# Performance work log

Measured on AMD Instinct MI355X. Metric: run time of the kernel, lower is better.

Reference implementation:

```python
import jax, jax.numpy as jnp
import numpy as np

B, N, KNN_K = 4, 4096, 32
C1, C = 128, 256
K_SLOTS, RECON_M, N_RECON = 4, 96, 128
SLOT_ITERS = 3

def _ln(x, g, b):
    m = x.mean(-1, keepdims=True)
    v = jnp.var(x, axis=-1, keepdims=True)
    return (x - m) * jax.lax.rsqrt(v + 1e-5) * g + b

def _gather(f, idx):
    # f [B,P,C], idx [B,N,K] -> [B,N,K,C]
    return jax.vmap(lambda a, i: a[i])(f, idx)

def _knn(xyz, k):
    sq = jnp.sum(xyz * xyz, -1)
    d = sq[:, :, None] + sq[:, None, :] - 2.0 * jnp.einsum('bnc,bmc->bnm', xyz, xyz)
    return jax.lax.top_k(-d, k)[1]

def _conv_block(xyz, feats, W, b):
    # InterZPConv-style: KNN neighbor gather -> per-neighbor transform -> max aggregate
    idx = _knn(xyz, KNN_K)
    rel = _gather(xyz, idx) - xyz[:, :, None, :]
    h = jnp.concatenate([_gather(feats, idx), rel], axis=-1)
    h = jax.nn.relu(jnp.einsum('bnkc,cd->bnkd', h, W) + b)
    return h.max(axis=2)

def _bn(x, g, b):
    # BatchNorm2d (training mode) over (batch, slot) axes for 1x1-conv stacks
    m = x.mean(axis=(0, 1), keepdims=True)
    v = jnp.var(x, axis=(0, 1), keepdims=True)
    return (x - m) * jax.lax.rsqrt(v + 1e-5) * g + b

def _gru(upd, prev, W_ih, W_hh, b_ih, b_hh):
    gi = upd @ W_ih + b_ih
    gh = prev @ W_hh + b_hh
    r = jax.nn.sigmoid(gi[..., :C] + gh[..., :C])
    z = jax.nn.sigmoid(gi[..., C:2 * C] + gh[..., C:2 * C])
    n = jnp.tanh(gi[..., 2 * C:] + r * gh[..., 2 * C:])
    return (1.0 - z) * n + z * prev

def _chamfer(a, b):
    # a [B,M,3], b [B,P,3] -> (min over b per a-point, min over a per b-point), squared dists
    d = jnp.sum((a[..., :, None, :] - b[..., None, :, :]) ** 2, axis=-1)
    return d.min(axis=-1), d.min(axis=-2)

def _fps(pts):
    # farthest point sampling of N_RECON points from pts [P,3]
    P = pts.shape[0]
    d0 = jnp.full((P,), 1e10, pts.dtype)
    def step(carry, _):
        d, last = carry
        d = jnp.minimum(d, jnp.sum((pts - pts[last]) ** 2, axis=-1))
        nxt = jnp.argmax(d).astype(jnp.int32)
        return (d, nxt), nxt
    _, idxs = jax.lax.scan(step, (d0, jnp.array(0, jnp.int32)), None, length=N_RECON - 1)
    return jnp.concatenate([jnp.zeros((1,), jnp.int32), idxs])

def setup_inputs() -> dict:
    key = jax.random.key(0)
    ks = jax.random.split(key, 16)
    w = lambda k, s: jax.random.normal(k, s, jnp.float32) * 0.02
    z = lambda *s: jnp.zeros(s, jnp.float32)
    o = lambda *s: jnp.ones(s, jnp.float32)
    return {
        'x': jax.random.normal(ks[0], (B, 3, N), jnp.float32),
        'pose': jnp.zeros((B, N, 4, 4), jnp.float32),
        'W1': w(ks[1], (1 + 3, C1)), 'b1': z(C1),
        'W2': w(ks[2], (C1 + 3, C)), 'b2': z(C),
        'slots_mu': w(ks[3], (1, 1, C)), 'slots_sigma': jnp.abs(w(ks[4], (1, 1, C))) + 0.01,
        'ln_in_g': o(C), 'ln_in_b': z(C),
        'ln_slot_g': o(C), 'ln_slot_b': z(C),
        'ln_ff_g': o(C), 'ln_ff_b': z(C),
        'Wq': w(ks[5], (C, C)), 'Wk': w(ks[6], (C, C)), 'Wv': w(ks[7], (C, C)),
        'W_ih': w(ks[8], (C, 3 * C)), 'W_hh': w(ks[9], (C, 3 * C)),
        'b_ih': z(3 * C), 'b_hh': z(3 * C),
        'Wm1': w(ks[10], (C, C)), 'bm1': z(C),
        'Wm2': w(ks[11], (C, C)), 'bm2': z(C),
        'Wr1': w(ks[12], (C, C)), 'br1': z(C), 'g1': o(C), 'be1': z(C),
        'Wr2': w(ks[13], (C, C)), 'br2': z(C), 'g2': o(C), 'be2': z(C),
        'Wr3': w(ks[14], (C, RECON_M * 3)), 'br3': z(RECON_M * 3),
    }

def reference(x, pose, W1, b1, W2, b2, slots_mu, slots_sigma, ln_in_g, ln_in_b,
              ln_slot_g, ln_slot_b, ln_ff_g, ln_ff_b, Wq, Wk, Wv,
              W_ih, W_hh, b_ih, b_hh, Wm1, bm1, Wm2, bm2,
              Wr1, br1, g1, be1, Wr2, br2, g2, be2, Wr3, br3):
    xyz = jnp.transpose(x, (0, 2, 1))  # [B,N,3]
    feats = jnp.ones((B, N, 1), x.dtype)  # preprocess_input: unit features, na=1
    f = _conv_block(xyz, feats, W1, b1)   # [B,N,C1]
    f = _conv_block(xyz, f, W2, b2)       # [B,N,C]
    # Slot attention over per-point invariant features
    inp = _ln(f, ln_in_g, ln_in_b)
    kk = inp @ Wk
    vv = inp @ Wv
    slots = slots_mu + slots_sigma * jax.random.normal(jax.random.key(42), (B, K_SLOTS, C), x.dtype)
    scale = C ** -0.5
    attn = None
    for _ in range(SLOT_ITERS):
        prev = slots
        q = _ln(slots, ln_slot_g, ln_slot_b) @ Wq
        logits = scale * jnp.einsum('bkc,bnc->bkn', q, kk)
        attn = jax.nn.softmax(logits, axis=1)  # softmax over slots
        wgt = attn / (attn.sum(axis=-1, keepdims=True) + 1e-8)
        upd = jnp.einsum('bkn,bnc->bkc', wgt, vv)
        slots = _gru(upd, prev, W_ih, W_hh, b_ih, b_hh)
        h = _ln(slots, ln_ff_g, ln_ff_b)
        slots = slots + (jax.nn.relu(h @ Wm1 + bm1) @ Wm2 + bm2)
    attn_out = jnp.transpose(attn, (0, 2, 1))  # [B,N,K] (attn_ori.transpose(1,2))
    # Part reconstruction net (1x1 conv + BN + ReLU stack on slot features)
    h = jax.nn.relu(_bn(slots @ Wr1 + br1, g1, be1))
    h = jax.nn.relu(_bn(h @ Wr2 + br2, g2, be2))
    slot_points = (h @ Wr3 + br3).reshape(B, K_SLOTS, RECON_M, 3)
    all_pts = slot_points.reshape(B, K_SLOTS * RECON_M, 3)
    # FPS downsample + global chamfer against input points
    idx = jax.vmap(_fps)(all_pts)  # [B, N_RECON]
    ds = jnp.take_along_axis(all_pts, idx[..., None], axis=1)  # [B,N_RECON,3]
    d1, d2 = _chamfer(ds, xyz)
    loss = (d1.mean(-1) + d2.mean(-1)).mean()
    return loss, attn_out
```

## Files before the change

### kernel.cpp

```cpp
#include <hip/hip_runtime.h>

#define NBATCH 4
#define NPTS   4096
#define KNNK   32
#define C1D    128
#define CD     256
#define KPAD   160
#define ASTR   168
#define ASTR2  264

typedef _Float16 v8h __attribute__((ext_vector_type(8)));
typedef float    v4f __attribute__((ext_vector_type(4)));
typedef unsigned long long ull;


__device__ __forceinline__ float block_sum256(float v, float* red) {
    #pragma unroll
    for (int o = 32; o; o >>= 1) v += __shfl_down(v, o);
    __syncthreads();
    if ((threadIdx.x & 63) == 0) red[threadIdx.x >> 6] = v;
    __syncthreads();
    return red[0] + red[1] + red[2] + red[3];
}

__device__ __forceinline__ unsigned rotl32(unsigned x, unsigned r) {
    return (x << r) | (x >> (32u - r));
}

__device__ float erfinv_f(float x) {
    float w = -log1pf(-x * x);
    float p;
    if (w < 5.0f) {
        w -= 2.5f;
        p = 2.81022636e-08f;
        p = fmaf(p, w, 3.43273939e-07f);
        p = fmaf(p, w, -3.5233877e-06f);
        p = fmaf(p, w, -4.39150654e-06f);
        p = fmaf(p, w, 0.00021858087f);
        p = fmaf(p, w, -0.00125372503f);
        p = fmaf(p, w, -0.00417768164f);
        p = fmaf(p, w, 0.246640727f);
        p = fmaf(p, w, 1.50140941f);
    } else {
        w = sqrtf(w) - 3.0f;
        p = -0.000200214257f;
        p = fmaf(p, w, 0.000100950558f);
        p = fmaf(p, w, 0.00134934322f);
        p = fmaf(p, w, -0.00367342844f);
        p = fmaf(p, w, 0.00573950773f);
        p = fmaf(p, w, -0.0076224613f);
        p = fmaf(p, w, 0.00943887047f);
        p = fmaf(p, w, 1.00167406f);
        p = fmaf(p, w, 2.83297682f);
    }
    return p * x;
}

__device__ __forceinline__ float bits_to_normal(unsigned bits) {
    unsigned fb = (bits >> 9) | 0x3f800000u;
    float f = __uint_as_float(fb) - 1.0f;
    const float lo = -0.99999994f;
    float u = fmaf(f, 2.0f, lo);
    u = fmaxf(u, lo);
    return 1.41421356237f * erfinv_f(u);
}

__device__ __forceinline__ unsigned fmap(float f) {
    unsigned b = __float_as_uint(f);
    return (b & 0x80000000u) ? ~b : (b | 0x80000000u);
}

template <int CTRL, int RM>
__device__ __forceinline__ ull dpp_min_u64(ull k) {
    unsigned lo = (unsigned)k, hi = (unsigned)(k >> 32);
    unsigned tlo = (unsigned)__builtin_amdgcn_update_dpp((int)lo, (int)lo, CTRL, RM, 0xf, false);
    unsigned thi = (unsigned)__builtin_amdgcn_update_dpp((int)hi, (int)hi, CTRL, RM, 0xf, false);
    ull t = ((ull)thi << 32) | tlo;
    return t < k ? t : k;
}

template <int CTRL, int RM>
__device__ __forceinline__ void dpp_lexmax(float& v, int& ix) {
    int tv = __builtin_amdgcn_update_dpp(__float_as_int(v), __float_as_int(v), CTRL, RM, 0xf, false);
    int ti = __builtin_amdgcn_update_dpp(ix, ix, CTRL, RM, 0xf, false);
    float fv = __int_as_float(tv);
    bool take = (fv > v) || (fv == v && ti < ix);
    v  = take ? fv : v;
    ix = take ? ti : ix;
}


__global__ __launch_bounds__(256) void prep_kernel(const float* __restrict__ x,
                                                   float* __restrict__ xyz,
                                                   float4* __restrict__ xyzw,
                                                   const float* __restrict__ mu,
                                                   const float* __restrict__ sg,
                                                   float* __restrict__ slots,
                                                   float* __restrict__ asum,
                                                   const float* __restrict__ W2,
                                                   const float* __restrict__ Wk,
                                                   const float* __restrict__ Wv,
                                                   _Float16* __restrict__ W2t,
                                                   _Float16* __restrict__ WkvT,
                                                   unsigned* __restrict__ counter) {
    int t = threadIdx.x;
    if (blockIdx.x < 64) {
        int gid = blockIdx.x * 256 + t;
        int b = gid >> 12, n = gid & (NPTS - 1);
        float a0 = x[(b * 3 + 0) * NPTS + n];
        float a1 = x[(b * 3 + 1) * NPTS + n];
        float a2 = x[(b * 3 + 2) * NPTS + n];
        xyz[gid * 3 + 0] = a0; xyz[gid * 3 + 1] = a1; xyz[gid * 3 + 2] = a2;
        float sq = a0 * a0 + a1 * a1 + a2 * a2;
        xyzw[gid] = make_float4(a0, a1, a2, sq);
        if (gid < 16) asum[gid] = 0.0f;
        if (gid == 16) counter[0] = 0u;
        if (gid < 2048) {
            int j = gid;
            unsigned ks0 = 0u, ks1 = 42u, ks2 = 0u ^ 42u ^ 0x1BD11BDAu;
            unsigned x0 = (unsigned)j + ks0;
            unsigned x1 = (unsigned)(j + 2048) + ks1;
            #define RND(r) { x0 += x1; x1 = rotl32(x1, r); x1 ^= x0; }
            RND(13u) RND(15u) RND(26u) RND(6u);  x0 += ks1; x1 += ks2 + 1u;
            RND(17u) RND(29u) RND(16u) RND(24u); x0 += ks2; x1 += ks0 + 2u;
            RND(13u) RND(15u) RND(26u) RND(6u);  x0 += ks0; x1 += ks1 + 3u;
            RND(17u) RND(29u) RND(16u) RND(24u); x0 += ks1; x1 += ks2 + 4u;
            RND(13u) RND(15u) RND(26u) RND(6u);  x0 += ks2; x1 += ks0 + 5u;
            #undef RND
            int c0 = j & 255, c1 = (j + 2048) & 255;
            slots[j]        = mu[c0] + sg[c0] * bits_to_normal(x0);
            slots[j + 2048] = mu[c1] + sg[c1] * bits_to_normal(x1);
        }
    } else if (blockIdx.x < 320) {
        int nb = blockIdx.x - 64;
        if (t < KPAD) W2t[nb * KPAD + t] = (t < 131) ? (_Float16)W2[t * CD + nb] : (_Float16)0.0f;
    } else {
        int n = blockIdx.x - 320;
        float v = (n < 256) ? Wk[t * CD + n] : Wv[t * CD + (n - 256)];
        WkvT[n * CD + t] = (_Float16)v;
    }
}

__global__ __launch_bounds__(256) void knn_kernel(const float4* __restrict__ xyzw,
                                                  int* __restrict__ knn_idx) {
    int wid = threadIdx.x >> 6, lane = threadIdx.x & 63;
    int pid = blockIdx.x * 4 + wid;
    int b = pid >> 12, n = pid & (NPTS - 1);
    const float4* xb = xyzw + (size_t)b * NPTS;
    float4 p = xb[n];
    unsigned d[64];
    #pragma unroll
    for (int i = 0; i < 64; ++i) {
        float4 c = xb[i * 64 + lane];
        float dot = p.x * c.x + p.y * c.y + p.z * c.z;
        d[i] = fmap(p.w + c.w - 2.0f * dot);
    }
    unsigned gv[8]; int gi[8];
    #pragma unroll
    for (int g = 0; g < 8; ++g) {
        unsigned mv = d[g * 8]; int mi = g * 8;
        #pragma unroll
        for (int j = 1; j < 8; ++j)
            if (d[g * 8 + j] < mv) { mv = d[g * 8 + j]; mi = g * 8 + j; }
        gv[g] = mv; gi[g] = mi * 64 + lane;
    }
    unsigned lv = gv[0]; int li = gi[0];
    #pragma unroll
    for (int g = 1; g < 8; ++g)
        if (gv[g] < lv) { lv = gv[g]; li = gi[g]; }

    int* out = knn_idx + (size_t)pid * KNNK;
    #pragma unroll 1
    for (int s = 0; s < KNNK; ++s) {
        ull k = ((ull)lv << 32) | (unsigned)li;
        k = dpp_min_u64<0x111, 0xf>(k);
        k = dpp_min_u64<0x112, 0xf>(k);
        k = dpp_min_u64<0x114, 0xf>(k);
        k = dpp_min_u64<0x118, 0xf>(k);
        k = dpp_min_u64<0x142, 0xa>(k);
        k = dpp_min_u64<0x143, 0xc>(k);
        int fm = __builtin_amdgcn_readlane((int)(unsigned)k, 63);
        if (lane == 0) out[s] = fm;
        int flane = fm & 63;
        int slot  = fm >> 6;
        if (lane == flane) {
            int g = slot >> 3;
            #pragma unroll
            for (int g2 = 0; g2 < 8; ++g2) {
                if (g2 == g) {
                    #pragma unroll
                    for (int j = 0; j < 8; ++j)
                        if (g2 * 8 + j == slot) d[g2 * 8 + j] = 0xFFFFFFFFu;
                    unsigned mv = d[g2 * 8]; int mi = g2 * 8;
                    #pragma unroll
                    for (int j = 1; j < 8; ++j)
                        if (d[g2 * 8 + j] < mv) { mv = d[g2 * 8 + j]; mi = g2 * 8 + j; }
                    gv[g2] = mv; gi[g2] = mi * 64 + lane;
                }
            }
            lv = gv[0]; li = gi[0];
            #pragma unroll
            for (int g2 = 1; g2 < 8; ++g2)
                if (gv[g2] < lv) { lv = gv[g2]; li = gi[g2]; }
        }
    }
}

__global__ __launch_bounds__(128) void conv1_kernel(const float* __restrict__ xyz,
                                                    const int* __restrict__ knn_idx,
                                                    const float* __restrict__ W1,
                                                    const float* __restrict__ b1,
                                                    _Float16* __restrict__ f1h) {
    int pid = blockIdx.x;
    int b = pid >> 12, n = pid & (NPTS - 1);
    int d = threadIdx.x, lane = threadIdx.x & 63;
    const float* xb = xyz + (size_t)b * NPTS * 3;
    float w0 = W1[d], wx = W1[C1D + d], wy = W1[2 * C1D + d], wz = W1[3 * C1D + d];
    float bb = b1[d];
    float px = xb[n * 3], py = xb[n * 3 + 1], pz = xb[n * 3 + 2];
    const int* idx = knn_idx + (size_t)pid * KNNK;
    float cx = 0.0f, cy = 0.0f, cz = 0.0f;
    if (lane < 32) {
        int j = idx[lane];
        cx = xb[j * 3]; cy = xb[j * 3 + 1]; cz = xb[j * 3 + 2];
    }
    float m = -1e30f;
    #pragma unroll
    for (int k = 0; k < KNNK; ++k) {
        float jx = __shfl(cx, k), jy = __shfl(cy, k), jz = __shfl(cz, k);
        float v = w0 + bb + (jx - px) * wx + (jy - py) * wy + (jz - pz) * wz;
        m = fmaxf(m, v);
    }
    f1h[(size_t)pid * C1D + d] = (_Float16)fmaxf(m, 0.0f);
}

__global__ __launch_bounds__(256) void conv2_mfma_kernel(const float* __restrict__ xyz,
                                                         const _Float16* __restrict__ f1h,
                                                         const int* __restrict__ knn_idx,
                                                         const _Float16* __restrict__ W2t,
                                                         const float* __restrict__ b2,
                                                         const float* __restrict__ g_in,
                                                         const float* __restrict__ b_in,
                                                         _Float16* __restrict__ inph) {
    __shared__ _Float16 A[64 * ASTR];
    __shared__ float colmax[2 * CD];
    __shared__ float red[4];
    int pid2 = blockIdx.x;
    int gp0 = pid2 * 2;
    int b = gp0 >> 12, n0 = gp0 & (NPTS - 1);
    int tid = threadIdx.x;
    const int* idx = knn_idx + (size_t)pid2 * 64;
    const float* xb = xyz + (size_t)b * NPTS * 3;

    {
        int r = tid & 63, seg = tid >> 6;
        int j = idx[r];
        const uint4* s4 = (const uint4*)(f1h + ((size_t)b * NPTS + j) * C1D);
        uint4* d4 = (uint4*)&A[r * ASTR];
        #pragma unroll
        for (int i = 0; i < 4; ++i) d4[seg * 4 + i] = s4[seg * 4 + i];
        unsigned* z = (unsigned*)&A[r * ASTR + 128];
        for (int i = seg; i < 20; i += 4) z[i] = 0u;
        int np_ = (r < 32) ? n0 : (n0 + 1);
        if (seg == 0) {
            A[r * ASTR + 128] = (_Float16)(xb[j * 3 + 0] - xb[np_ * 3 + 0]);
            A[r * ASTR + 129] = (_Float16)(xb[j * 3 + 1] - xb[np_ * 3 + 1]);
        } else if (seg == 1) {
            A[r * ASTR + 130] = (_Float16)(xb[j * 3 + 2] - xb[np_ * 3 + 2]);
        }
    }
    __syncthreads();

    int w = tid >> 6, lane = tid & 63, quad = lane >> 4, lr = lane & 15;
    v4f acc[4][4];
    #pragma unroll
    for (int rt = 0; rt < 4; ++rt)
        #pragma unroll
        for (int ct = 0; ct < 4; ++ct)
            acc[rt][ct] = (v4f){0.0f, 0.0f, 0.0f, 0.0f};

    #pragma unroll
    for (int kk = 0; kk < KPAD; kk += 32) {
        v8h af[4], bf[4];
        #pragma unroll
        for (int rt = 0; rt < 4; ++rt)
            af[rt] = *(const v8h*)&A[(rt * 16 + lr) * ASTR + kk + quad * 8];
        #pragma unroll
        for (int ct = 0; ct < 4; ++ct) {
            int ncol = w * 64 + ct * 16 + lr;
            bf[ct] = *(const v8h*)(W2t + (size_t)ncol * KPAD + kk + quad * 8);
        }
        #pragma unroll
        for (int rt = 0; rt < 4; ++rt)
            #pragma unroll
            for (int ct = 0; ct < 4; ++ct)
                acc[rt][ct] = __builtin_amdgcn_mfma_f32_16x16x32_f16(af[rt], bf[ct], acc[rt][ct], 0, 0, 0);
    }

    #pragma unroll
    for (int ct = 0; ct < 4; ++ct) {
        float tm[4];
        #pragma unroll
        for (int rt = 0; rt < 4; ++rt) {
            v4f a = acc[rt][ct];
            float v = fmaxf(fmaxf(a[0], a[1]), fmaxf(a[2], a[3]));
            v = fmaxf(v, __shfl_xor(v, 16));
            v = fmaxf(v, __shfl_xor(v, 32));
            tm[rt] = v;
        }
        float p0 = fmaxf(tm[0], tm[1]);
        float p1 = fmaxf(tm[2], tm[3]);
        if (quad == 0) {
            colmax[0 * CD + w * 64 + ct * 16 + lr] = p0;
            colmax[1 * CD + w * 64 + ct * 16 + lr] = p1;
        }
    }
    __syncthreads();

    int d = tid;
    #pragma unroll
    for (int p = 0; p < 2; ++p) {
        float v = fmaxf(colmax[p * CD + d] + b2[d], 0.0f);
        float s = block_sum256(v, red);
        float mean = s * (1.0f / 256.0f);
        float s2 = block_sum256(v * v, red);
        float var = s2 * (1.0f / 256.0f) - mean * mean;
        float iv = (v - mean) * rsqrtf(var + 1e-5f) * g_in[d] + b_in[d];
        inph[(size_t)(gp0 + p) * CD + d] = (_Float16)iv;
    }
}

__global__ __launch_bounds__(256) void kv_mfma_kernel(const _Float16* __restrict__ inph,
                                                      const _Float16* __restrict__ WkvT,
                                                      float* __restrict__ kk,
                                                      float* __restrict__ vv) {
    __shared__ _Float16 A[64 * ASTR2];
    int rb = blockIdx.x >> 1, half = blockIdx.x & 1;
    int row0 = rb * 64;
    int tid = threadIdx.x;
    {
        const uint4* src4 = (const uint4*)(inph + (size_t)row0 * CD);
        #pragma unroll
        for (int i = 0; i < 8; ++i) {
            int idx = i * 256 + tid;
            int row = idx >> 5, c8 = idx & 31;
            *(uint4*)&A[row * ASTR2 + c8 * 8] = src4[idx];
        }
    }
    __syncthreads();
    int w = tid >> 6, lane = tid & 63, quad = lane >> 4, lr = lane & 15;
    v4f acc[4][4];
    #pragma unroll
    for (int rt = 0; rt < 4; ++rt)
        #pragma unroll
        for (int ct = 0; ct < 4; ++ct)
            acc[rt][ct] = (v4f){0.0f, 0.0f, 0.0f, 0.0f};
    #pragma unroll
    for (int ks = 0; ks < CD; ks += 32) {
        v8h af[4], bf[4];
        #pragma unroll
        for (int rt = 0; rt < 4; ++rt)
            af[rt] = *(const v8h*)&A[(rt * 16 + lr) * ASTR2 + ks + quad * 8];
        #pragma unroll
        for (int ct = 0; ct < 4; ++ct) {
            int ncol = half * 256 + w * 64 + ct * 16 + lr;
            bf[ct] = *(const v8h*)(WkvT + (size_t)ncol * CD + ks + quad * 8);
        }
        #pragma unroll
        for (int rt = 0; rt < 4; ++rt)
            #pragma unroll
            for (int ct = 0; ct < 4; ++ct)
                acc[rt][ct] = __builtin_amdgcn_mfma_f32_16x16x32_f16(af[rt], bf[ct], acc[rt][ct], 0, 0, 0);
    }
    float* dst = half ? vv : kk;
    #pragma unroll
    for (int rt = 0; rt < 4; ++rt)
        #pragma unroll
        for (int ct = 0; ct < 4; ++ct) {
            int col = w * 64 + ct * 16 + lr;
            #pragma unroll
            for (int r = 0; r < 4; ++r) {
                int row = rt * 16 + quad * 4 + r;
                dst[(size_t)(row0 + row) * CD + col] = acc[rt][ct][r];
            }
        }
}

__global__ __launch_bounds__(256) void slotq_kernel(const float* __restrict__ slots,
                                                    const float* __restrict__ g_sl,
                                                    const float* __restrict__ b_sl,
                                                    const float* __restrict__ Wq,
                                                    float* __restrict__ q) {
    int row = blockIdx.x;
    int d = threadIdx.x;
    __shared__ float sl[CD];
    __shared__ float red[4];
    float v = slots[row * CD + d];
    float s = block_sum256(v, red);
    float mean = s * (1.0f / 256.0f);
    float s2 = block_sum256(v * v, red);
    float var = s2 * (1.0f / 256.0f) - mean * mean;
    float ln = (v - mean) * rsqrtf(var + 1e-5f) * g_sl[d] + b_sl[d];
    sl[d] = ln;
    __syncthreads();
    float acc = 0.0f;
    const float4* sp = (const float4*)sl;
    for (int c4 = 0; c4 < 64; ++c4) {
        float4 x = sp[c4];
        int cb = c4 * 4;
        acc += x.x * Wq[cb * CD + d] + x.y * Wq[(cb + 1) * CD + d]
             + x.z * Wq[(cb + 2) * CD + d] + x.w * Wq[(cb + 3) * CD + d];
    }
    q[row * CD + d] = acc;
}

__global__ __launch_bounds__(256) void attn_updp_kernel(const float* __restrict__ q,
                                                        const float* __restrict__ kk,
                                                        const float* __restrict__ vv,
                                                        float* __restrict__ asum,
                                                        float* __restrict__ updp,
                                                        float* __restrict__ out_attn) {
    int b = blockIdx.x >> 6;
    int chunk = blockIdx.x & 63;
    int t = threadIdx.x;
    __shared__ float qs[4 * CD];
    __shared__ float logit[64 * 4];
    __shared__ float aw[64 * 4];
    for (int i = t; i < 4 * CD; i += 256) qs[i] = q[b * 4 * CD + i];
    __syncthreads();

    int p = t & 63, r = t >> 6;
    int n = chunk * 64 + p;
    {
        const float4* kp = (const float4*)(kk + ((size_t)b * NPTS + n) * CD);
        const float4* qr = (const float4*)(qs + r * CD);
        float a = 0.0f;
        for (int c4 = 0; c4 < 64; ++c4) {
            float4 kv = kp[c4];
            float4 x = qr[c4];
            a += kv.x * x.x + kv.y * x.y + kv.z * x.z + kv.w * x.w;
        }
        logit[p * 4 + r] = 0.0625f * a;
    }
    __syncthreads();
    if (t < 64) {
        float l0 = logit[t * 4 + 0], l1 = logit[t * 4 + 1];
        float l2 = logit[t * 4 + 2], l3 = logit[t * 4 + 3];
        float mx = fmaxf(fmaxf(l0, l1), fmaxf(l2, l3));
        float e0 = expf(l0 - mx), e1 = expf(l1 - mx), e2 = expf(l2 - mx), e3 = expf(l3 - mx);
        float inv = 1.0f / (e0 + e1 + e2 + e3);
        e0 *= inv; e1 *= inv; e2 *= inv; e3 *= inv;
        aw[t * 4 + 0] = e0; aw[t * 4 + 1] = e1; aw[t * 4 + 2] = e2; aw[t * 4 + 3] = e3;
        if (out_attn) {
            float* o = out_attn + ((size_t)b * NPTS + chunk * 64 + t) * 4;
            o[0] = e0; o[1] = e1; o[2] = e2; o[3] = e3;
        }
        float s0 = e0, s1 = e1, s2 = e2, s3 = e3;
        #pragma unroll
        for (int o = 32; o; o >>= 1) {
            s0 += __shfl_down(s0, o); s1 += __shfl_down(s1, o);
            s2 += __shfl_down(s2, o); s3 += __shfl_down(s3, o);
        }
        if (t == 0) {
            atomicAdd(&asum[b * 4 + 0], s0);
            atomicAdd(&asum[b * 4 + 1], s1);
            atomicAdd(&asum[b * 4 + 2], s2);
            atomicAdd(&asum[b * 4 + 3], s3);
        }
    }
    __syncthreads();

    float ac0 = 0.0f, ac1 = 0.0f, ac2 = 0.0f, ac3 = 0.0f;
    const float* vb = vv + ((size_t)b * NPTS + chunk * 64) * CD;
    for (int nn2 = 0; nn2 < 64; ++nn2) {
        float v = vb[(size_t)nn2 * CD + t];
        float4 w4 = *(const float4*)&aw[nn2 * 4];
        ac0 += w4.x * v; ac1 += w4.y * v; ac2 += w4.z * v; ac3 += w4.w * v;
    }
    updp[((size_t)(b * 4 + 0) * 64 + chunk) * CD + t] = ac0;
    updp[((size_t)(b * 4 + 1) * 64 + chunk) * CD + t] = ac1;
    updp[((size_t)(b * 4 + 2) * 64 + chunk) * CD + t] = ac2;
    updp[((size_t)(b * 4 + 3) * 64 + chunk) * CD + t] = ac3;
}

__global__ __launch_bounds__(256) void gru_gates_kernel(const float* __restrict__ updp,
                                                        const float* __restrict__ asum,
                                                        const float* __restrict__ slots,
                                                        const float* __restrict__ W_ih,
                                                        const float* __restrict__ W_hh,
                                                        const float* __restrict__ b_ih,
                                                        const float* __restrict__ b_hh,
                                                        float* __restrict__ gi,
                                                        float* __restrict__ gh) {
    int idx = blockIdx.x;
    int row = idx / 6, rem = idx % 6;
    int gate = rem >> 1, half = rem & 1;
    int d = threadIdx.x;
    __shared__ float su[CD], sp[CD];
    float f = 1.0f / (asum[row] + 1e-8f);
    float u = 0.0f;
    for (int p = 0; p < 64; ++p) u += updp[((size_t)row * 64 + p) * CD + d];
    u *= f;
    su[d] = u; sp[d] = slots[row * CD + d];
    __syncthreads();
    float acc_i = half ? 0.0f : b_ih[gate * CD + d];
    float acc_h = half ? 0.0f : b_hh[gate * CD + d];
    const float* wi = W_ih + gate * CD + d;
    const float* wh = W_hh + gate * CD + d;
    int c0 = half * 128;
    for (int c = c0; c < c0 + 128; ++c) {
        acc_i += su[c] * wi[c * 3 * CD];
        acc_h += sp[c] * wh[c * 3 * CD];
    }
    gi[((size_t)(row * 3 + gate) * 2 + half) * CD + d] = acc_i;
    gh[((size_t)(row * 3 + gate) * 2 + half) * CD + d] = acc_h;
}

__global__ __launch_bounds__(256) void gru_mlp_kernel(const float* __restrict__ gi,
                                                      const float* __restrict__ gh,
                                                      float* __restrict__ slots,
                                                      const float* __restrict__ g_ff,
                                                      const float* __restrict__ b_ff,
                                                      const float* __restrict__ Wm1,
                                                      const float* __restrict__ bm1,
                                                      const float* __restrict__ Wm2,
                                                      const float* __restrict__ bm2,
                                                      float* __restrict__ asum,
                                                      const float* __restrict__ g_sl,
                                                      const float* __restrict__ b_sl,
                                                      const float* __restrict__ Wq,
                                                      float* __restrict__ qv) {
    int row = blockIdx.x;
    int d = threadIdx.x;
    __shared__ float sh[CD];
    __shared__ float red[4];
    float prev = slots[row * CD + d];
    float gir = gi[((size_t)(row * 3 + 0) * 2 + 0) * CD + d] + gi[((size_t)(row * 3 + 0) * 2 + 1) * CD + d];
    float giz = gi[((size_t)(row * 3 + 1) * 2 + 0) * CD + d] + gi[((size_t)(row * 3 + 1) * 2 + 1) * CD + d];
    float gin = gi[((size_t)(row * 3 + 2) * 2 + 0) * CD + d] + gi[((size_t)(row * 3 + 2) * 2 + 1) * CD + d];
    float ghr = gh[((size_t)(row * 3 + 0) * 2 + 0) * CD + d] + gh[((size_t)(row * 3 + 0) * 2 + 1) * CD + d];
    float ghz = gh[((size_t)(row * 3 + 1) * 2 + 0) * CD + d] + gh[((size_t)(row * 3 + 1) * 2 + 1) * CD + d];
    float ghn = gh[((size_t)(row * 3 + 2) * 2 + 0) * CD + d] + gh[((size_t)(row * 3 + 2) * 2 + 1) * CD + d];
    if (d == 0) asum[row] = 0.0f;
    float r = 1.0f / (1.0f + expf(-(gir + ghr)));
    float z = 1.0f / (1.0f + expf(-(giz + ghz)));
    float nn = tanhf(gin + r * ghn);
    float sNew = (1.0f - z) * nn + z * prev;
    float s = block_sum256(sNew, red);
    float mean = s * (1.0f / 256.0f);
    float s2 = block_sum256(sNew * sNew, red);
    float var = s2 * (1.0f / 256.0f) - mean * mean;
    float h = (sNew - mean) * rsqrtf(var + 1e-5f) * g_ff[d] + b_ff[d];
    __syncthreads();
    sh[d] = h;
    __syncthreads();
    float y = bm1[d];
    {
        const float4* hp = (const float4*)sh;
        for (int c4 = 0; c4 < 64; ++c4) {
            float4 x = hp[c4];
            int cb = c4 * 4;
            y += x.x * Wm1[cb * CD + d] + x.y * Wm1[(cb + 1) * CD + d]
               + x.z * Wm1[(cb + 2) * CD + d] + x.w * Wm1[(cb + 3) * CD + d];
        }
    }
    y = fmaxf(y, 0.0f);
    __syncthreads();
    sh[d] = y;
    __syncthreads();
    float o = bm2[d];
    {
        const float4* hp = (const float4*)sh;
        for (int c4 = 0; c4 < 64; ++c4) {
            float4 x = hp[c4];
            int cb = c4 * 4;
            o += x.x * Wm2[cb * CD + d] + x.y * Wm2[(cb + 1) * CD + d]
               + x.z * Wm2[(cb + 2) * CD + d] + x.w * Wm2[(cb + 3) * CD + d];
        }
    }
    float fin = sNew + o;
    slots[row * CD + d] = fin;
    if (qv) {
        float v = fin;
        float s3 = block_sum256(v, red);
        float mean2 = s3 * (1.0f / 256.0f);
        float s4 = block_sum256(v * v, red);
        float var2 = s4 * (1.0f / 256.0f) - mean2 * mean2;
        float ln = (v - mean2) * rsqrtf(var2 + 1e-5f) * g_sl[d] + b_sl[d];
        __syncthreads();
        sh[d] = ln;
        __syncthreads();
        float acc = 0.0f;
        const float4* sp = (const float4*)sh;
        for (int c4 = 0; c4 < 64; ++c4) {
            float4 x = sp[c4];
            int cb = c4 * 4;
            acc += x.x * Wq[cb * CD + d] + x.y * Wq[(cb + 1) * CD + d]
                 + x.z * Wq[(cb + 2) * CD + d] + x.w * Wq[(cb + 3) * CD + d];
        }
        qv[row * CD + d] = acc;
    }
}

__global__ __launch_bounds__(320) void recon_fps_kernel(const float* __restrict__ slots,
                                                        const float* __restrict__ Wr1, const float* __restrict__ br1,
                                                        const float* __restrict__ g1, const float* __restrict__ be1,
                                                        const float* __restrict__ Wr2, const float* __restrict__ br2,
                                                        const float* __restrict__ g2, const float* __restrict__ be2,
                                                        const float* __restrict__ Wr3, const float* __restrict__ br3,
                                                        float* __restrict__ spts,
                                                        int* __restrict__ fidx,
                                                        float* __restrict__ lacc,
                                                        unsigned* __restrict__ mnbuf) {
    __shared__ float sl[16 * CD];
    __shared__ float h1[16 * CD];
    __shared__ float h2[16 * CD];
    __shared__ float sp[384 * 3];
    int b = blockIdx.x;
    int d = threadIdx.x;
    if (d < CD) for (int r = 0; r < 16; ++r) sl[r * CD + d] = slots[r * CD + d];
    __syncthreads();
    if (d < CD) {
        float t[16];
        #pragma unroll
        for (int r = 0; r < 16; ++r) t[r] = br1[d];
        for (int c4 = 0; c4 < 64; ++c4) {
            int cb = c4 * 4;
            float w0 = Wr1[cb * CD + d], w1 = Wr1[(cb + 1) * CD + d];
            float w2 = Wr1[(cb + 2) * CD + d], w3 = Wr1[(cb + 3) * CD + d];
            #pragma unroll
            for (int r = 0; r < 16; ++r) {
                float4 x = *(const float4*)(sl + r * CD + cb);
                t[r] += x.x * w0 + x.y * w1 + x.z * w2 + x.w * w3;
            }
        }
        float mean = 0.0f;
        for (int r = 0; r < 16; ++r) mean += t[r];
        mean *= (1.0f / 16.0f);
        float var = 0.0f;
        for (int r = 0; r < 16; ++r) { float dd = t[r] - mean; var += dd * dd; }
        var *= (1.0f / 16.0f);
        float inv = rsqrtf(var + 1e-5f);
        for (int r = 0; r < 16; ++r)
            h1[r * CD + d] = fmaxf(0.0f, (t[r] - mean) * inv * g1[d] + be1[d]);
    }
    __syncthreads();
    if (d < CD) {
        float t[16];
        #pragma unroll
        for (int r = 0; r < 16; ++r) t[r] = br2[d];
        for (int c4 = 0; c4 < 64; ++c4) {
            int cb = c4 * 4;
            float w0 = Wr2[cb * CD + d], w1 = Wr2[(cb + 1) * CD + d];
            float w2 = Wr2[(cb + 2) * CD + d], w3 = Wr2[(cb + 3) * CD + d];
            #pragma unroll
            for (int r = 0; r < 16; ++r) {
                float4 x = *(const float4*)(h1 + r * CD + cb);
                t[r] += x.x * w0 + x.y * w1 + x.z * w2 + x.w * w3;
            }
        }
        float mean = 0.0f;
        for (int r = 0; r < 16; ++r) mean += t[r];
        mean *= (1.0f / 16.0f);
        float var = 0.0f;
        for (int r = 0; r < 16; ++r) { float dd = t[r] - mean; var += dd * dd; }
        var *= (1.0f / 16.0f);
        float inv = rsqrtf(var + 1e-5f);
        for (int r = 0; r < 16; ++r)
            h2[r * CD + d] = fmaxf(0.0f, (t[r] - mean) * inv * g2[d] + be2[d]);
    }
    __syncthreads();
    if (d < 288) {
        #pragma unroll
        for (int rl = 0; rl < 4; ++rl) {
            int r = b * 4 + rl;
            float t = br3[d];
            for (int c4 = 0; c4 < 64; ++c4) {
                int cb = c4 * 4;
                float w0 = Wr3[cb * 288 + d], w1 = Wr3[(cb + 1) * 288 + d];
                float w2 = Wr3[(cb + 2) * 288 + d], w3 = Wr3[(cb + 3) * 288 + d];
                float4 x = *(const float4*)(h2 + r * CD + cb);
                t += x.x * w0 + x.y * w1 + x.z * w2 + x.w * w3;
            }
            spts[r * 288 + d] = t;
            sp[rl * 288 + d] = t;
        }
    }
    __syncthreads();

    if (d < 64) {
        int lane = d;
        int* out = fidx + b * 128;
        if (lane == 0) out[0] = 0;
        if (b == 0 && lane == 0) lacc[0] = 0.0f;
        mnbuf[b * 128 + lane] = 0x7F800000u;
        mnbuf[b * 128 + 64 + lane] = 0x7F800000u;
        float px[6], py[6], pz[6], dd[6];
        #pragma unroll
        for (int i = 0; i < 6; ++i) {
            int m = i * 64 + lane;
            px[i] = sp[m * 3]; py[i] = sp[m * 3 + 1]; pz[i] = sp[m * 3 + 2];
            dd[i] = 1e10f;
        }
        float lx = sp[0], ly = sp[1], lz = sp[2];
        #pragma unroll 1
        for (int s = 1; s < 128; ++s) {
            #pragma unroll
            for (int i = 0; i < 6; ++i) {
                float dx = px[i] - lx, dy = py[i] - ly, dz = pz[i] - lz;
                dd[i] = fminf(dd[i], dx * dx + dy * dy + dz * dz);
            }
            float bv = dd[0]; int bi = lane;
            #pragma unroll
            for (int i = 1; i < 6; ++i)
                if (dd[i] > bv) { bv = dd[i]; bi = i * 64 + lane; }
            dpp_lexmax<0x111, 0xf>(bv, bi);
            dpp_lexmax<0x112, 0xf>(bv, bi);
            dpp_lexmax<0x114, 0xf>(bv, bi);
            dpp_lexmax<0x118, 0xf>(bv, bi);
            dpp_lexmax<0x142, 0xa>(bv, bi);
            dpp_lexmax<0x143, 0xc>(bv, bi);
            int fm = __builtin_amdgcn_readlane(bi, 63);
            if (lane == 0) out[s] = fm;
            int slot = fm >> 6, sl_lane = fm & 63;
            float sx = px[0], sy = py[0], sz = pz[0];
            #pragma unroll
            for (int i = 1; i < 6; ++i)
                if (slot == i) { sx = px[i]; sy = py[i]; sz = pz[i]; }
            lx = __int_as_float(__builtin_amdgcn_readlane(__float_as_int(sx), sl_lane));
            ly = __int_as_float(__builtin_amdgcn_readlane(__float_as_int(sy), sl_lane));
            lz = __int_as_float(__builtin_amdgcn_readlane(__float_as_int(sz), sl_lane));
        }
    }
}

__global__ __launch_bounds__(256) void chamfer_kernel(const float* __restrict__ spts,
                                                      const int* __restrict__ fidx,
                                                      const float* __restrict__ xyz,
                                                      float* __restrict__ lacc,
                                                      unsigned* __restrict__ mnbuf,
                                                      unsigned* __restrict__ counter,
                                                      float* __restrict__ out) {
    int t = threadIdx.x;
    __shared__ float ds[128 * 3];
    __shared__ float tile[256 * 3];
    __shared__ float red[4];
    __shared__ unsigned done;
    if (blockIdx.x < 64) {
        int b = blockIdx.x >> 4, chunk = blockIdx.x & 15;
        const float* pts = spts + (size_t)b * 384 * 3;
        if (t < 128) {
            int j = fidx[b * 128 + t];
            ds[t * 3] = pts[j * 3]; ds[t * 3 + 1] = pts[j * 3 + 1]; ds[t * 3 + 2] = pts[j * 3 + 2];
        }
        __syncthreads();
        int n = chunk * 256 + t;
        const float* xb = xyz + (size_t)b * NPTS * 3;
        float px = xb[n * 3], py = xb[n * 3 + 1], pz = xb[n * 3 + 2];
        float mn = 1e30f;
        #pragma unroll 4
        for (int jj = 0; jj < 128; ++jj) {
            float dx = ds[jj * 3] - px, dy = ds[jj * 3 + 1] - py, dz = ds[jj * 3 + 2] - pz;
            mn = fminf(mn, dx * dx + dy * dy + dz * dz);
        }
        float total = block_sum256(mn * (1.0f / 4096.0f), red);
        if (t == 0) atomicAdd(lacc, total);
    } else {
        int bid = blockIdx.x - 64;
        int b = bid >> 4, chunk = bid & 15;
        const float* xb = xyz + ((size_t)b * NPTS + chunk * 256) * 3;
        for (int i = t; i < 768; i += 256) tile[i] = xb[i];
        __syncthreads();
        if (t < 128) {
            int j = fidx[b * 128 + t];
            const float* pts = spts + (size_t)b * 384 * 3;
            float px = pts[j * 3], py = pts[j * 3 + 1], pz = pts[j * 3 + 2];
            float mn = 1e30f;
            #pragma unroll 4
            for (int i = 0; i < 256; ++i) {
                float dx = tile[i * 3] - px, dy = tile[i * 3 + 1] - py, dz = tile[i * 3 + 2] - pz;
                mn = fminf(mn, dx * dx + dy * dy + dz * dz);
            }
            atomicMin(&mnbuf[b * 128 + t], __float_as_uint(mn));
        }
    }
    __threadfence();
    __syncthreads();
    if (t == 0) done = atomicAdd(counter, 1u);
    __syncthreads();
    if (done == 127u) {
        unsigned a0 = atomicAdd(&mnbuf[t], 0u);
        unsigned a1 = atomicAdd(&mnbuf[t + 256], 0u);
        float v = (__uint_as_float(a0) + __uint_as_float(a1)) * (1.0f / 128.0f);
        __syncthreads();
        float tot = block_sum256(v, red);
        if (t == 0) {
            float l = atomicAdd(lacc, 0.0f);
            out[0] = (l + tot) * 0.25f;
        }
    }
}


extern "C" void kernel_launch(void* const* d_in, const int* in_sizes, int n_in,
                              void* d_out, int out_size, void* d_ws, size_t ws_size,
                              hipStream_t stream) {
    (void)in_sizes; (void)n_in; (void)out_size; (void)ws_size;
    const float* x    = (const float*)d_in[0];
    const float* W1   = (const float*)d_in[2];
    const float* b1   = (const float*)d_in[3];
    const float* W2   = (const float*)d_in[4];
    const float* b2   = (const float*)d_in[5];
    const float* mu   = (const float*)d_in[6];
    const float* sg   = (const float*)d_in[7];
    const float* g_in = (const float*)d_in[8];
    const float* b_in = (const float*)d_in[9];
    const float* g_sl = (const float*)d_in[10];
    const float* b_sl = (const float*)d_in[11];
    const float* g_ff = (const float*)d_in[12];
    const float* b_ff = (const float*)d_in[13];
    const float* Wq   = (const float*)d_in[14];
    const float* Wk   = (const float*)d_in[15];
    const float* Wv   = (const float*)d_in[16];
    const float* W_ih = (const float*)d_in[17];
    const float* W_hh = (const float*)d_in[18];
    const float* b_ih = (const float*)d_in[19];
    const float* b_hh = (const float*)d_in[20];
    const float* Wm1  = (const float*)d_in[21];
    const float* bm1  = (const float*)d_in[22];
    const float* Wm2  = (const float*)d_in[23];
    const float* bm2  = (const float*)d_in[24];
    const float* Wr1  = (const float*)d_in[25];
    const float* br1  = (const float*)d_in[26];
    const float* g1   = (const float*)d_in[27];
    const float* be1  = (const float*)d_in[28];
    const float* Wr2  = (const float*)d_in[29];
    const float* br2  = (const float*)d_in[30];
    const float* g2   = (const float*)d_in[31];
    const float* be2  = (const float*)d_in[32];
    const float* Wr3  = (const float*)d_in[33];
    const float* br3  = (const float*)d_in[34];

    float* ws    = (float*)d_ws;
    float* xyz   = ws;
    float* xyzw  = xyz + 49152;
    int*   knn   = (int*)(xyzw + 65536);
    _Float16* f1h = (_Float16*)(knn + 524288);
    _Float16* W2t = (_Float16*)((float*)f1h + 1048576);
    _Float16* WkvT = (_Float16*)((float*)W2t + 20480);
    _Float16* inph = (_Float16*)((float*)WkvT + 65536);
    float* kkb   = (float*)inph + 2097152;
    float* vvb   = kkb + 4194304;
    float* slots = vvb + 4194304;
    float* qb    = slots + 4096;
    float* asum  = qb + 4096;
    float* updp  = asum + 16;
    float* gi    = updp + 262144;
    float* gh    = gi + 24576;
    float* spts  = gh + 24576;
    int*   fidx  = (int*)(spts + 4608);
    float* lacc  = (float*)(fidx + 512);
    unsigned* mnbuf = (unsigned*)(lacc + 1);
    unsigned* counter = mnbuf + 512;

    float* out = (float*)d_out;

    prep_kernel<<<832, 256, 0, stream>>>(x, xyz, (float4*)xyzw, mu, sg, slots, asum,
                                         W2, Wk, Wv, W2t, WkvT, counter);
    knn_kernel<<<NBATCH * NPTS / 4, 256, 0, stream>>>((const float4*)xyzw, knn);
    conv1_kernel<<<NBATCH * NPTS, 128, 0, stream>>>(xyz, knn, W1, b1, f1h);
    conv2_mfma_kernel<<<NBATCH * NPTS / 2, 256, 0, stream>>>(xyz, f1h, knn, W2t, b2, g_in, b_in, inph);
    kv_mfma_kernel<<<NBATCH * NPTS / 64 * 2, 256, 0, stream>>>(inph, WkvT, kkb, vvb);

    slotq_kernel<<<16, 256, 0, stream>>>(slots, g_sl, b_sl, Wq, qb);
    for (int it = 0; it < 3; ++it) {
        attn_updp_kernel<<<256, 256, 0, stream>>>(qb, kkb, vvb, asum, updp,
                                                  (it == 2) ? (out + 1) : (float*)nullptr);
        gru_gates_kernel<<<96, 256, 0, stream>>>(updp, asum, slots, W_ih, W_hh, b_ih, b_hh, gi, gh);
        gru_mlp_kernel<<<16, 256, 0, stream>>>(gi, gh, slots, g_ff, b_ff, Wm1, bm1, Wm2, bm2, asum,
                                               g_sl, b_sl, Wq, (it < 2) ? qb : (float*)nullptr);
    }

    recon_fps_kernel<<<4, 320, 0, stream>>>(slots, Wr1, br1, g1, be1, Wr2, br2, g2, be2,
                                            Wr3, br3, spts, fidx, lacc, mnbuf);
    chamfer_kernel<<<128, 256, 0, stream>>>(spts, fidx, xyz, lacc, mnbuf, counter, out);
}
```

Baseline: 692.2 us.

## Split recon MLP layers into separate multi-block kernels before FPS

Before, each of 4 blocks recomputed the two 256x256 BN+ReLU layers for all 16 slot rows redundantly. Now each layer runs as its own 16-block kernel, with each thread computing one output element and the batch-norm statistics taken through shared memory. The third layer and FPS stay in a 4-block kernel that reads h2 from global memory. This removes the redundant serial work and spreads it over more compute units, at the cost of two extra kernel launches and a global round trip.

```diff
diff --git a/kernel.cpp b/kernel.cpp
--- a/kernel.cpp
+++ b/kernel.cpp
@@ -602,88 +602,70 @@
     }
 }
 
-__global__ __launch_bounds__(320) void recon_fps_kernel(const float* __restrict__ slots,
-                                                        const float* __restrict__ Wr1, const float* __restrict__ br1,
-                                                        const float* __restrict__ g1, const float* __restrict__ be1,
-                                                        const float* __restrict__ Wr2, const float* __restrict__ br2,
-                                                        const float* __restrict__ g2, const float* __restrict__ be2,
-                                                        const float* __restrict__ Wr3, const float* __restrict__ br3,
-                                                        float* __restrict__ spts,
-                                                        int* __restrict__ fidx,
-                                                        float* __restrict__ lacc,
-                                                        unsigned* __restrict__ mnbuf) {
-    __shared__ float sl[16 * CD];
-    __shared__ float h1[16 * CD];
+__global__ __launch_bounds__(256) void recon_layer_kernel(const float* __restrict__ in,
+                                                          const float* __restrict__ W,
+                                                          const float* __restrict__ bias,
+                                                          const float* __restrict__ g,
+                                                          const float* __restrict__ be,
+                                                          float* __restrict__ outb) {
+    __shared__ float sin[16 * CD];
+    __shared__ float tb[16 * 16];
+    int t = threadIdx.x;
+    for (int i = t; i < 16 * CD; i += 256) sin[i] = in[i];
+    __syncthreads();
+    int col = t & 15, row = t >> 4;
+    int colg = blockIdx.x * 16 + col;
+    float acc = bias[colg];
+    for (int c4 = 0; c4 < 64; ++c4) {
+        int cb = c4 * 4;
+        float w0 = W[cb * CD + colg], w1 = W[(cb + 1) * CD + colg];
+        float w2 = W[(cb + 2) * CD + colg], w3 = W[(cb + 3) * CD + colg];
+        float4 x = *(const float4*)(sin + row * CD + cb);
+        acc += x.x * w0 + x.y * w1 + x.z * w2 + x.w * w3;
+    }
+    tb[row * 16 + col] = acc;
+    __syncthreads();
+    float mean = 0.0f;
+    for (int r = 0; r < 16; ++r) mean += tb[r * 16 + col];
+    mean *= (1.0f / 16.0f);
+    float var = 0.0f;
+    for (int r = 0; r < 16; ++r) { float dd = tb[r * 16 + col] - mean; var += dd * dd; }
+    var *= (1.0f / 16.0f);
+    float inv = rsqrtf(var + 1e-5f);
+    outb[row * CD + colg] = fmaxf(0.0f, (acc - mean) * inv * g[colg] + be[colg]);
+}
+
+__global__ __launch_bounds__(320) void recon3_fps_kernel(const float* __restrict__ h2g,
+                                                         const float* __restrict__ Wr3,
+                                                         const float* __restrict__ br3,
+                                                         float* __restrict__ spts,
+                                                         int* __restrict__ fidx,
+                                                         float* __restrict__ lacc,
+                                                         unsigned* __restrict__ mnbuf) {
     __shared__ float h2[16 * CD];
     __shared__ float sp[384 * 3];
     int b = blockIdx.x;
     int d = threadIdx.x;
-    if (d < CD) for (int r = 0; r < 16; ++r) sl[r * CD + d] = slots[r * CD + d];
-    __syncthreads();
-    if (d < CD) {
-        float t[16];
-        #pragma unroll
-        for (int r = 0; r < 16; ++r) t[r] = br1[d];
+    for (int i = d; i < 16 * CD; i += 320) h2[i] = h2g[i];
+    __syncthreads();
+    if (d < 288) {
+        float t4[4];
+        #pragma unroll
+        for (int rl = 0; rl < 4; ++rl) t4[rl] = br3[d];
         for (int c4 = 0; c4 < 64; ++c4) {
             int cb = c4 * 4;
-            float w0 = Wr1[cb * CD + d], w1 = Wr1[(cb + 1) * CD + d];
-            float w2 = Wr1[(cb + 2) * CD + d], w3 = Wr1[(cb + 3) * CD + d];
+            float w0 = Wr3[cb * 288 + d], w1 = Wr3[(cb + 1) * 288 + d];
+            float w2 = Wr3[(cb + 2) * 288 + d], w3 = Wr3[(cb + 3) * 288 + d];
             #pragma unroll
-            for (int r = 0; r < 16; ++r) {
-                float4 x = *(const float4*)(sl + r * CD + cb);
-                t[r] += x.x * w0 + x.y * w1 + x.z * w2 + x.w * w3;
+            for (int rl = 0; rl < 4; ++rl) {
+                float4 x = *(const float4*)(h2 + (b * 4 + rl) * CD + cb);
+                t4[rl] += x.x * w0 + x.y * w1 + x.z * w2 + x.w * w3;
             }
         }
-        float mean = 0.0f;
-        for (int r = 0; r < 16; ++r) mean += t[r];
-        mean *= (1.0f / 16.0f);
-        float var = 0.0f;
-        for (int r = 0; r < 16; ++r) { float dd = t[r] - mean; var += dd * dd; }
-        var *= (1.0f / 16.0f);
-        float inv = rsqrtf(var + 1e-5f);
-        for (int r = 0; r < 16; ++r)
-            h1[r * CD + d] = fmaxf(0.0f, (t[r] - mean) * inv * g1[d] + be1[d]);
-    }
-    __syncthreads();
-    if (d < CD) {
-        float t[16];
-        #pragma unroll
-        for (int r = 0; r < 16; ++r) t[r] = br2[d];
-        for (int c4 = 0; c4 < 64; ++c4) {
-            int cb = c4 * 4;
-            float w0 = Wr2[cb * CD + d], w1 = Wr2[(cb + 1) * CD + d];
-            float w2 = Wr2[(cb + 2) * CD + d], w3 = Wr2[(cb + 3) * CD + d];
-            #pragma unroll
-            for (int r = 0; r < 16; ++r) {
-                float4 x = *(const float4*)(h1 + r * CD + cb);
-                t[r] += x.x * w0 + x.y * w1 + x.z * w2 + x.w * w3;
-            }
-        }
-        float mean = 0.0f;
-        for (int r = 0; r < 16; ++r) mean += t[r];
-        mean *= (1.0f / 16.0f);
-        float var = 0.0f;
-        for (int r = 0; r < 16; ++r) { float dd = t[r] - mean; var += dd * dd; }
-        var *= (1.0f / 16.0f);
-        float inv = rsqrtf(var + 1e-5f);
-        for (int r = 0; r < 16; ++r)
-            h2[r * CD + d] = fmaxf(0.0f, (t[r] - mean) * inv * g2[d] + be2[d]);
-    }
-    __syncthreads();
-    if (d < 288) {
         #pragma unroll
         for (int rl = 0; rl < 4; ++rl) {
-            int r = b * 4 + rl;
-            float t = br3[d];
-            for (int c4 = 0; c4 < 64; ++c4) {
-                int cb = c4 * 4;
-                float w0 = Wr3[cb * 288 + d], w1 = Wr3[(cb + 1) * 288 + d];
-                float w2 = Wr3[(cb + 2) * 288 + d], w3 = Wr3[(cb + 3) * 288 + d];
-                float4 x = *(const float4*)(h2 + r * CD + cb);
-                t += x.x * w0 + x.y * w1 + x.z * w2 + x.w * w3;
-            }
-            spts[r * 288 + d] = t;
-            sp[rl * 288 + d] = t;
+            spts[(b * 4 + rl) * 288 + d] = t4[rl];
+            sp[rl * 288 + d] = t4[rl];
         }
     }
     __syncthreads();
@@ -857,7 +839,9 @@
     float* updp  = asum + 16;
     float* gi    = updp + 262144;
     float* gh    = gi + 24576;
-    float* spts  = gh + 24576;
+    float* h1g   = gh + 24576;
+    float* h2g   = h1g + 4096;
+    float* spts  = h2g + 4096;
     int*   fidx  = (int*)(spts + 4608);
     float* lacc  = (float*)(fidx + 512);
     unsigned* mnbuf = (unsigned*)(lacc + 1);
@@ -881,7 +865,8 @@
                                                g_sl, b_sl, Wq, (it < 2) ? qb : (float*)nullptr);
     }
 
-    recon_fps_kernel<<<4, 320, 0, stream>>>(slots, Wr1, br1, g1, be1, Wr2, br2, g2, be2,
-                                            Wr3, br3, spts, fidx, lacc, mnbuf);
+    recon_layer_kernel<<<16, 256, 0, stream>>>(slots, Wr1, br1, g1, be1, h1g);
+    recon_layer_kernel<<<16, 256, 0, stream>>>(h1g, Wr2, br2, g2, be2, h2g);
+    recon3_fps_kernel<<<4, 320, 0, stream>>>(h2g, Wr3, br3, spts, fidx, lacc, mnbuf);
     chamfer_kernel<<<128, 256, 0, stream>>>(spts, fidx, xyz, lacc, mnbuf, counter, out);
 }
```

Result: faster. 678.5 us (-2.0%).
